# Kernel optimization log

Measured on AMD Instinct MI355X. Metric: run time of the kernel, lower is better.

## Reference

```python
import jax, jax.numpy as jnp
import numpy as np

N_NODES = 100000
N_EDGES = 3200000
IN_SIZE = 256
HID_SIZE = 256
OUT_SIZE = 64


def setup_inputs() -> dict:
    key = jax.random.key(0)
    ks = jax.random.split(key, 8)
    X = jax.random.normal(ks[0], (N_NODES, IN_SIZE), dtype=jnp.float32)
    edge_vals = jax.random.uniform(ks[1], (N_EDGES,), dtype=jnp.float32)
    # xavier-uniform-ish init for weights
    lim1 = float(np.sqrt(6.0 / (IN_SIZE + HID_SIZE)))
    W1 = jax.random.uniform(ks[2], (IN_SIZE, HID_SIZE), minval=-lim1, maxval=lim1, dtype=jnp.float32)
    b1 = jnp.zeros((HID_SIZE,), dtype=jnp.float32)
    lim2 = float(np.sqrt(6.0 / (HID_SIZE + OUT_SIZE)))
    W2 = jax.random.uniform(ks[3], (HID_SIZE, OUT_SIZE), minval=-lim2, maxval=lim2, dtype=jnp.float32)
    b2 = jnp.zeros((OUT_SIZE,), dtype=jnp.float32)
    row = jnp.sort(jax.random.randint(ks[4], (N_EDGES,), 0, N_NODES, dtype=jnp.int32))
    col = jax.random.randint(ks[5], (N_EDGES,), 0, N_NODES, dtype=jnp.int32)
    return {"X": X, "edge_vals": edge_vals, "W1": W1, "b1": b1,
            "W2": W2, "b2": b2, "row": row, "col": col}


def reference(X, edge_vals, W1, b1, W2, b2, row, col):
    """2-layer GCN (eval mode, dropout = identity).

    A is a sparse NxN matrix in COO form: A[row[e], col[e]] = edge_vals[e].
    Layer: relu(A @ (X @ W1) + b1); output: A @ (h @ W2) + b2.
    """
    n = X.shape[0]

    def spmm(dense):  # (A @ dense): gather columns, scale, segment-sum over rows
        gathered = edge_vals[:, None] * dense[col]        # [E, F]
        return jax.ops.segment_sum(gathered, row, num_segments=n)

    h = spmm(X @ W1) + b1          # [N, HID]
    h = jax.nn.relu(h)
    out = spmm(h @ W2) + b2        # [N, OUT]
    return out
```

## Files before the change

kernel.cpp:

```cpp
#include <hip/hip_runtime.h>


constexpr int IN_SIZE = 256;
constexpr int HID = 256;
constexpr int OUTF = 64;

typedef __bf16 bf16x8 __attribute__((ext_vector_type(8)));
typedef float f32x4 __attribute__((ext_vector_type(4)));

__device__ __forceinline__ ushort f2b(float f) {
    uint u = __float_as_uint(f);
    uint r = (u + 0x7fffu + ((u >> 16) & 1u)) >> 16;
    return (ushort)r;
}

__device__ __forceinline__ void fma4(float* a, uint word, float w) {
    a[0] += w * (float)(word & 0xffu);
    a[1] += w * (float)((word >> 8) & 0xffu);
    a[2] += w * (float)((word >> 16) & 0xffu);
    a[3] += w * (float)(word >> 24);
}

__device__ __forceinline__ bf16x8 pack8(float4 a, float4 b) {
    union { uint4 u; bf16x8 h; } cv;
    cv.u.x = (uint)f2b(a.x) | ((uint)f2b(a.y) << 16);
    cv.u.y = (uint)f2b(a.z) | ((uint)f2b(a.w) << 16);
    cv.u.z = (uint)f2b(b.x) | ((uint)f2b(b.y) << 16);
    cv.u.w = (uint)f2b(b.z) | ((uint)f2b(b.w) << 16);
    return cv.h;
}

__global__ void setup_kernel(const int* __restrict__ row, int* __restrict__ rp,
                             const float* __restrict__ W1, ushort* __restrict__ W1T,
                             const float* __restrict__ W2, ushort* __restrict__ W2T,
                             int n, int E, int rpB) {
    int b = blockIdx.x;
    if (b < rpB) {
        int i = b * 256 + threadIdx.x;
        if (i > n) return;
        int lo = 0, hi = E;
        while (lo < hi) {
            int mid = (lo + hi) >> 1;
            if (row[mid] < i) lo = mid + 1; else hi = mid;
        }
        rp[i] = lo;
    } else if (b < rpB + 256) {
        int nn = b - rpB;
        int k = threadIdx.x;
        W1T[(size_t)nn * 256 + k] = f2b(W1[(size_t)k * 256 + nn]);
    } else {
        int nn = b - rpB - 256;
        int k = threadIdx.x;
        W2T[(size_t)nn * 256 + k] = f2b(W2[(size_t)k * 64 + nn]);
    }
}

__global__ void prep_edges(const float* __restrict__ vals, const int* __restrict__ col,
                           const float* __restrict__ s, int2* __restrict__ ew,
                           int E, int shift) {
    int e = blockIdx.x * 256 + threadIdx.x;
    if (e >= E) return;
    int c = col[e];
    ew[e] = make_int2(c << shift, __float_as_int(vals[e] * s[c]));
}

__global__ __launch_bounds__(512)
void gemm1_q(const float* __restrict__ A, const ushort* __restrict__ Bt,
             unsigned char* __restrict__ Q, float* __restrict__ s1, int M) {
    __shared__ uint4 Wlds[8192];
    const int tid = threadIdx.x;
    const int wave = tid >> 6, lane = tid & 63;
    const int quad = lane >> 4, l = lane & 15;
    const int wr = wave >> 2, wc = wave & 3;
    const int m0 = blockIdx.x * 128;

    for (int i = tid; i < 8192; i += 512) {
        uint4 v = ((const uint4*)Bt)[i];
        Wlds[(i & ~31) | ((i & 31) ^ ((i >> 5) & 7))] = v;
    }
    __syncthreads();

    size_t abase[4];
#pragma unroll
    for (int mt = 0; mt < 4; ++mt) {
        int r = min(m0 + wr * 64 + mt * 16 + l, M - 1);
        abase[mt] = (size_t)r * 256 + quad * 8;
    }

    f32x4 acc[4][4] = {};
    float4 ra[4], rb[4];
#pragma unroll
    for (int mt = 0; mt < 4; ++mt) {
        ra[mt] = *(const float4*)(A + abase[mt]);
        rb[mt] = *(const float4*)(A + abase[mt] + 4);
    }

#pragma unroll
    for (int kstep = 0; kstep < 8; ++kstep) {
        bf16x8 af[4];
#pragma unroll
        for (int mt = 0; mt < 4; ++mt)
            af[mt] = pack8(ra[mt], rb[mt]);
        if (kstep < 7) {
#pragma unroll
            for (int mt = 0; mt < 4; ++mt) {
                ra[mt] = *(const float4*)(A + abase[mt] + (kstep + 1) * 32);
                rb[mt] = *(const float4*)(A + abase[mt] + (kstep + 1) * 32 + 4);
            }
        }
        bf16x8 bfr[4];
#pragma unroll
        for (int nt = 0; nt < 4; ++nt) {
            int c = wc * 64 + nt * 16 + l;
            int idx = c * 32 + (((kstep << 2) + quad) ^ (c & 7));
            bfr[nt] = *(const bf16x8*)&Wlds[idx];
        }
#pragma unroll
        for (int mt = 0; mt < 4; ++mt)
#pragma unroll
            for (int nt = 0; nt < 4; ++nt)
                acc[mt][nt] = __builtin_amdgcn_mfma_f32_16x16x32_bf16(
                    af[mt], bfr[nt], acc[mt][nt], 0, 0, 0);
    }

    __syncthreads();
    float* red = (float*)Wlds;
    float* fin = red + 512;

    float rmax[4][4];
#pragma unroll
    for (int mt = 0; mt < 4; ++mt)
#pragma unroll
        for (int reg = 0; reg < 4; ++reg) {
            float m = 0.f;
#pragma unroll
            for (int nt = 0; nt < 4; ++nt)
                m = fmaxf(m, fabsf(acc[mt][nt][reg]));
            rmax[mt][reg] = m;
        }
#pragma unroll
    for (int s = 1; s <= 8; s <<= 1)
#pragma unroll
        for (int mt = 0; mt < 4; ++mt)
#pragma unroll
            for (int reg = 0; reg < 4; ++reg)
                rmax[mt][reg] = fmaxf(rmax[mt][reg], __shfl_xor(rmax[mt][reg], s));
    if (l < 4) {
#pragma unroll
        for (int mt = 0; mt < 4; ++mt)
            red[wc * 128 + wr * 64 + mt * 16 + quad * 4 + l] = rmax[mt][l];
    }
    __syncthreads();
    if (tid < 128) {
        float m = fmaxf(fmaxf(red[tid], red[128 + tid]),
                        fmaxf(red[256 + tid], red[384 + tid]));
        fin[tid] = m;
        int r = m0 + tid;
        if (r < M) s1[r] = m * (1.f / 127.f);
    }
    __syncthreads();

#pragma unroll
    for (int mt = 0; mt < 4; ++mt)
#pragma unroll
        for (int reg = 0; reg < 4; ++reg) {
            int rl = wr * 64 + mt * 16 + quad * 4 + reg;
            int r = m0 + rl;
            if (r >= M) continue;
            float m = fin[rl];
            float inv = m > 0.f ? 127.f / m : 0.f;
#pragma unroll
            for (int nt = 0; nt < 4; ++nt) {
                int c = wc * 64 + nt * 16 + l;
                Q[(size_t)r * 256 + c] =
                    (unsigned char)((int)rintf(acc[mt][nt][reg] * inv) + 128);
            }
        }
}

__global__ __launch_bounds__(256, 4)
void gemm2_q(const ushort* __restrict__ A, const ushort* __restrict__ Bt,
             unsigned char* __restrict__ Q, float* __restrict__ s2, int M) {
    __shared__ uint4 Wlds[2048];
    const int tid = threadIdx.x;
    const int wave = tid >> 6, lane = tid & 63;
    const int quad = lane >> 4, l = lane & 15;
    const int r0 = blockIdx.x * 128 + wave * 32;

    for (int i = tid; i < 2048; i += 256) {
        uint4 v = ((const uint4*)Bt)[i];
        Wlds[(i & ~31) | ((i & 31) ^ ((i >> 5) & 7))] = v;
    }
    __syncthreads();

    size_t abase[2];
#pragma unroll
    for (int mt = 0; mt < 2; ++mt) {
        int r = min(r0 + mt * 16 + l, M - 1);
        abase[mt] = (size_t)r * 256 + quad * 8;
    }

    f32x4 acc[2][4] = {};
    uint4 ra[2];
#pragma unroll
    for (int mt = 0; mt < 2; ++mt)
        ra[mt] = *(const uint4*)(A + abase[mt]);

#pragma unroll
    for (int kstep = 0; kstep < 8; ++kstep) {
        bf16x8 af[2];
#pragma unroll
        for (int mt = 0; mt < 2; ++mt)
            af[mt] = *(const bf16x8*)&ra[mt];
        if (kstep < 7) {
#pragma unroll
            for (int mt = 0; mt < 2; ++mt)
                ra[mt] = *(const uint4*)(A + abase[mt] + (kstep + 1) * 32);
        }
        bf16x8 bfr[4];
#pragma unroll
        for (int nt = 0; nt < 4; ++nt) {
            int c = nt * 16 + l;
            int idx = c * 32 + (((kstep << 2) + quad) ^ (c & 7));
            bfr[nt] = *(const bf16x8*)&Wlds[idx];
        }
#pragma unroll
        for (int mt = 0; mt < 2; ++mt)
#pragma unroll
            for (int nt = 0; nt < 4; ++nt)
                acc[mt][nt] = __builtin_amdgcn_mfma_f32_16x16x32_bf16(
                    af[mt], bfr[nt], acc[mt][nt], 0, 0, 0);
    }

    float rmax[2][4];
#pragma unroll
    for (int mt = 0; mt < 2; ++mt)
#pragma unroll
        for (int reg = 0; reg < 4; ++reg) {
            float m = fmaxf(fabsf(acc[mt][0][reg]), fabsf(acc[mt][1][reg]));
            m = fmaxf(m, fabsf(acc[mt][2][reg]));
            m = fmaxf(m, fabsf(acc[mt][3][reg]));
            rmax[mt][reg] = m;
        }
#pragma unroll
    for (int s = 1; s <= 8; s <<= 1)
#pragma unroll
        for (int mt = 0; mt < 2; ++mt)
#pragma unroll
            for (int reg = 0; reg < 4; ++reg)
                rmax[mt][reg] = fmaxf(rmax[mt][reg], __shfl_xor(rmax[mt][reg], s));

#pragma unroll
    for (int mt = 0; mt < 2; ++mt)
#pragma unroll
        for (int reg = 0; reg < 4; ++reg) {
            int r = r0 + mt * 16 + quad * 4 + reg;
            if (r >= M) continue;
            float m = rmax[mt][reg];
            if (l == 0) s2[r] = m * (1.f / 127.f);
            float inv = m > 0.f ? 127.f / m : 0.f;
#pragma unroll
            for (int nt = 0; nt < 4; ++nt) {
                int c = nt * 16 + l;
                Q[(size_t)r * 64 + c] =
                    (unsigned char)((int)rintf(acc[mt][nt][reg] * inv) + 128);
            }
        }
}

__global__ __launch_bounds__(256)
void spmm1_q(const unsigned char* __restrict__ Q, const int2* __restrict__ ew,
             const int* __restrict__ rp, const float* __restrict__ bias,
             ushort* __restrict__ H, int n) {
    const int wave = threadIdx.x >> 6;
    const int lane = threadIdx.x & 63;
    const int node = blockIdx.x * 4 + wave;
    if (node >= n) return;
    const int e0 = rp[node], e1 = rp[node + 1];
    const int g = lane >> 4;
    const int fb = (lane & 15) * 16;

    float acc[16] = {};
    float sumw = 0.f;
    int e = e0;
    for (; e + 16 <= e1; e += 16) {
#pragma unroll
        for (int u = 0; u < 4; ++u) {
            int2 m = ew[e + u * 4 + g];
            float w = __int_as_float(m.y);
            uint4 qv = *(const uint4*)(Q + (size_t)(uint)m.x + fb);
            sumw += w;
            fma4(&acc[0], qv.x, w);
            fma4(&acc[4], qv.y, w);
            fma4(&acc[8], qv.z, w);
            fma4(&acc[12], qv.w, w);
        }
    }
    for (; e < e1; e += 4) {
        int idx = e + g;
        int2 m = ew[idx];
        bool ok = idx < e1;
        uint off = ok ? (uint)m.x : 0u;
        float w = ok ? __int_as_float(m.y) : 0.f;
        uint4 qv = *(const uint4*)(Q + (size_t)off + fb);
        sumw += w;
        fma4(&acc[0], qv.x, w);
        fma4(&acc[4], qv.y, w);
        fma4(&acc[8], qv.z, w);
        fma4(&acc[12], qv.w, w);
    }

#pragma unroll
    for (int s = 16; s <= 32; s <<= 1) {
#pragma unroll
        for (int j = 0; j < 16; ++j)
            acc[j] += __shfl_xor(acc[j], s);
        sumw += __shfl_xor(sumw, s);
    }

    if (g == 0) {
        const int f0 = (lane & 15) * 16;
        float4 b0 = *(const float4*)(bias + f0);
        float4 b1 = *(const float4*)(bias + f0 + 4);
        float4 b2 = *(const float4*)(bias + f0 + 8);
        float4 b3 = *(const float4*)(bias + f0 + 12);
        float bb[16] = {b0.x, b0.y, b0.z, b0.w, b1.x, b1.y, b1.z, b1.w,
                        b2.x, b2.y, b2.z, b2.w, b3.x, b3.y, b3.z, b3.w};
        float fix = -128.f * sumw;
        ushort r[16];
#pragma unroll
        for (int j = 0; j < 16; ++j)
            r[j] = f2b(fmaxf(acc[j] + fix + bb[j], 0.f));
        uint4 w0, w1;
        w0.x = (uint)r[0] | ((uint)r[1] << 16);
        w0.y = (uint)r[2] | ((uint)r[3] << 16);
        w0.z = (uint)r[4] | ((uint)r[5] << 16);
        w0.w = (uint)r[6] | ((uint)r[7] << 16);
        w1.x = (uint)r[8] | ((uint)r[9] << 16);
        w1.y = (uint)r[10] | ((uint)r[11] << 16);
        w1.z = (uint)r[12] | ((uint)r[13] << 16);
        w1.w = (uint)r[14] | ((uint)r[15] << 16);
        *(uint4*)(H + (size_t)node * 256 + f0) = w0;
        *(uint4*)(H + (size_t)node * 256 + f0 + 8) = w1;
    }
}

__global__ __launch_bounds__(256)
void spmm2_q(const unsigned char* __restrict__ Q, const int2* __restrict__ ew,
             const int* __restrict__ rp, const float* __restrict__ bias,
             float* __restrict__ O, int n) {
    const int wave = threadIdx.x >> 6;
    const int lane = threadIdx.x & 63;
    const int node = blockIdx.x * 4 + wave;
    if (node >= n) return;
    const int e0 = rp[node], e1 = rp[node + 1];
    const int g = lane >> 3;
    const int fb = (lane & 7) * 8;

    float acc[8] = {};
    float sumw = 0.f;
    int e = e0;
    for (; e + 16 <= e1; e += 16) {
#pragma unroll
        for (int u = 0; u < 2; ++u) {
            int2 m = ew[e + u * 8 + g];
            float w = __int_as_float(m.y);
            uint2 qv = *(const uint2*)(Q + (size_t)(uint)m.x + fb);
            sumw += w;
            fma4(&acc[0], qv.x, w);
            fma4(&acc[4], qv.y, w);
        }
    }
    for (; e < e1; e += 8) {
        int idx = e + g;
        int2 m = ew[idx];
        bool ok = idx < e1;
        uint off = ok ? (uint)m.x : 0u;
        float w = ok ? __int_as_float(m.y) : 0.f;
        uint2 qv = *(const uint2*)(Q + (size_t)off + fb);
        sumw += w;
        fma4(&acc[0], qv.x, w);
        fma4(&acc[4], qv.y, w);
    }

#pragma unroll
    for (int s = 8; s <= 32; s <<= 1) {
#pragma unroll
        for (int j = 0; j < 8; ++j)
            acc[j] += __shfl_xor(acc[j], s);
        sumw += __shfl_xor(sumw, s);
    }

    if (g == 0) {
        const int f0 = (lane & 7) * 8;
        float4 b0 = *(const float4*)(bias + f0);
        float4 b1 = *(const float4*)(bias + f0 + 4);
        float fix = -128.f * sumw;
        float4 o0, o1;
        o0.x = acc[0] + fix + b0.x;
        o0.y = acc[1] + fix + b0.y;
        o0.z = acc[2] + fix + b0.z;
        o0.w = acc[3] + fix + b0.w;
        o1.x = acc[4] + fix + b1.x;
        o1.y = acc[5] + fix + b1.y;
        o1.z = acc[6] + fix + b1.z;
        o1.w = acc[7] + fix + b1.w;
        *(float4*)(O + (size_t)node * 64 + f0) = o0;
        *(float4*)(O + (size_t)node * 64 + f0 + 4) = o1;
    }
}

static inline size_t alignup(size_t x) { return (x + 255) & ~(size_t)255; }

extern "C" void kernel_launch(void* const* d_in, const int* in_sizes, int n_in,
                              void* d_out, int out_size, void* d_ws, size_t ws_size,
                              hipStream_t stream) {
    const float* X  = (const float*)d_in[0];
    const float* ev = (const float*)d_in[1];
    const float* W1 = (const float*)d_in[2];
    const float* b1 = (const float*)d_in[3];
    const float* W2 = (const float*)d_in[4];
    const float* b2 = (const float*)d_in[5];
    const int*  row = (const int*)d_in[6];
    const int*  col = (const int*)d_in[7];
    float* out = (float*)d_out;

    const int n = in_sizes[0] / IN_SIZE;
    const int E = in_sizes[1];

    char* p = (char*)d_ws;
    ushort* H    = (ushort*)p; p += alignup((size_t)n * HID * 2);
    unsigned char* Q1 = (unsigned char*)p; p += alignup((size_t)n * HID);
    float*  s1   = (float*)p;  p += alignup((size_t)n * 4);
    unsigned char* Q2 = (unsigned char*)p; p += alignup((size_t)n * OUTF);
    float*  s2   = (float*)p;  p += alignup((size_t)n * 4);
    ushort* W1T  = (ushort*)p; p += alignup((size_t)IN_SIZE * HID * 2);
    ushort* W2T  = (ushort*)p; p += alignup((size_t)HID * OUTF * 2);
    int*    rp   = (int*)p;    p += alignup((size_t)(n + 1) * 4);
    int2*   ewb  = (int2*)p;   p += alignup((size_t)(E + 16) * 8);

    const int rpB = (n + 1 + 255) / 256;
    setup_kernel<<<rpB + 256 + 64, 256, 0, stream>>>(row, rp, W1, W1T, W2, W2T,
                                                     n, E, rpB);

    gemm1_q<<<(n + 127) / 128, 512, 0, stream>>>(X, W1T, Q1, s1, n);

    prep_edges<<<(E + 255) / 256, 256, 0, stream>>>(ev, col, s1, ewb, E, 8);

    spmm1_q<<<(n + 3) / 4, 256, 0, stream>>>(Q1, ewb, rp, b1, H, n);

    gemm2_q<<<(n + 127) / 128, 256, 0, stream>>>(H, W2T, Q2, s2, n);

    prep_edges<<<(E + 255) / 256, 256, 0, stream>>>(ev, col, s2, ewb, E, 6);

    spmm2_q<<<(n + 3) / 4, 256, 0, stream>>>(Q2, ewb, rp, b2, out, n);
}
```

Before: 484.5 us.

## Retile gemm1 to 1024-thread blocks, deepen A prefetch, split spmm1 launch

gemm1_q now uses 1024-thread blocks covering 256 rows, with each wave computing a 32x128 tile instead of 64x64. The W1 LDS load is amortized over twice as many rows, and B fragments are loaded one at a time to reduce register pressure. Both GEMMs now prefetch A two k-steps ahead to hide global load latency. spmm1 is split into two launches over node halves, which adds a launch with no clear benefit, possibly for cache locality or as an experiment.

```diff
diff --git a/kernel.cpp b/kernel.cpp
--- a/kernel.cpp
+++ b/kernel.cpp
@@ -64,96 +64,96 @@
     ew[e] = make_int2(c << shift, __float_as_int(vals[e] * s[c]));
 }
 
-__global__ __launch_bounds__(512)
+__global__ __launch_bounds__(1024)
 void gemm1_q(const float* __restrict__ A, const ushort* __restrict__ Bt,
              unsigned char* __restrict__ Q, float* __restrict__ s1, int M) {
     __shared__ uint4 Wlds[8192];
     const int tid = threadIdx.x;
     const int wave = tid >> 6, lane = tid & 63;
     const int quad = lane >> 4, l = lane & 15;
-    const int wr = wave >> 2, wc = wave & 3;
-    const int m0 = blockIdx.x * 128;
-
-    for (int i = tid; i < 8192; i += 512) {
+    const int wr = wave >> 1, wc = wave & 1;
+    const int m0 = blockIdx.x * 256;
+
+    for (int i = tid; i < 8192; i += 1024) {
         uint4 v = ((const uint4*)Bt)[i];
         Wlds[(i & ~31) | ((i & 31) ^ ((i >> 5) & 7))] = v;
     }
     __syncthreads();
 
-    size_t abase[4];
-#pragma unroll
-    for (int mt = 0; mt < 4; ++mt) {
-        int r = min(m0 + wr * 64 + mt * 16 + l, M - 1);
+    size_t abase[2];
+#pragma unroll
+    for (int mt = 0; mt < 2; ++mt) {
+        int r = min(m0 + wr * 32 + mt * 16 + l, M - 1);
         abase[mt] = (size_t)r * 256 + quad * 8;
     }
 
-    f32x4 acc[4][4] = {};
-    float4 ra[4], rb[4];
-#pragma unroll
-    for (int mt = 0; mt < 4; ++mt) {
-        ra[mt] = *(const float4*)(A + abase[mt]);
-        rb[mt] = *(const float4*)(A + abase[mt] + 4);
+    f32x4 acc[2][8] = {};
+    float4 ra0[2], rb0[2], ra1[2], rb1[2];
+#pragma unroll
+    for (int mt = 0; mt < 2; ++mt) {
+        ra0[mt] = *(const float4*)(A + abase[mt]);
+        rb0[mt] = *(const float4*)(A + abase[mt] + 4);
+        ra1[mt] = *(const float4*)(A + abase[mt] + 32);
+        rb1[mt] = *(const float4*)(A + abase[mt] + 36);
     }
 
 #pragma unroll
     for (int kstep = 0; kstep < 8; ++kstep) {
-        bf16x8 af[4];
-#pragma unroll
-        for (int mt = 0; mt < 4; ++mt)
-            af[mt] = pack8(ra[mt], rb[mt]);
-        if (kstep < 7) {
-#pragma unroll
-            for (int mt = 0; mt < 4; ++mt) {
-                ra[mt] = *(const float4*)(A + abase[mt] + (kstep + 1) * 32);
-                rb[mt] = *(const float4*)(A + abase[mt] + (kstep + 1) * 32 + 4);
+        bf16x8 af[2];
+#pragma unroll
+        for (int mt = 0; mt < 2; ++mt)
+            af[mt] = pack8(ra0[mt], rb0[mt]);
+#pragma unroll
+        for (int mt = 0; mt < 2; ++mt) { ra0[mt] = ra1[mt]; rb0[mt] = rb1[mt]; }
+        if (kstep < 6) {
+#pragma unroll
+            for (int mt = 0; mt < 2; ++mt) {
+                ra1[mt] = *(const float4*)(A + abase[mt] + (kstep + 2) * 32);
+                rb1[mt] = *(const float4*)(A + abase[mt] + (kstep + 2) * 32 + 4);
             }
         }
-        bf16x8 bfr[4];
-#pragma unroll
-        for (int nt = 0; nt < 4; ++nt) {
-            int c = wc * 64 + nt * 16 + l;
+#pragma unroll
+        for (int nt = 0; nt < 8; ++nt) {
+            int c = wc * 128 + nt * 16 + l;
             int idx = c * 32 + (((kstep << 2) + quad) ^ (c & 7));
-            bfr[nt] = *(const bf16x8*)&Wlds[idx];
-        }
-#pragma unroll
-        for (int mt = 0; mt < 4; ++mt)
-#pragma unroll
-            for (int nt = 0; nt < 4; ++nt)
+            bf16x8 bfr = *(const bf16x8*)&Wlds[idx];
+#pragma unroll
+            for (int mt = 0; mt < 2; ++mt)
                 acc[mt][nt] = __builtin_amdgcn_mfma_f32_16x16x32_bf16(
-                    af[mt], bfr[nt], acc[mt][nt], 0, 0, 0);
+                    af[mt], bfr, acc[mt][nt], 0, 0, 0);
+        }
     }
 
     __syncthreads();
     float* red = (float*)Wlds;
     float* fin = red + 512;
 
-    float rmax[4][4];
-#pragma unroll
-    for (int mt = 0; mt < 4; ++mt)
+    float rmax[2][4];
+#pragma unroll
+    for (int mt = 0; mt < 2; ++mt)
 #pragma unroll
         for (int reg = 0; reg < 4; ++reg) {
             float m = 0.f;
 #pragma unroll
-            for (int nt = 0; nt < 4; ++nt)
+            for (int nt = 0; nt < 8; ++nt)
                 m = fmaxf(m, fabsf(acc[mt][nt][reg]));
             rmax[mt][reg] = m;
         }
 #pragma unroll
     for (int s = 1; s <= 8; s <<= 1)
 #pragma unroll
-        for (int mt = 0; mt < 4; ++mt)
+        for (int mt = 0; mt < 2; ++mt)
 #pragma unroll
             for (int reg = 0; reg < 4; ++reg)
                 rmax[mt][reg] = fmaxf(rmax[mt][reg], __shfl_xor(rmax[mt][reg], s));
     if (l < 4) {
 #pragma unroll
-        for (int mt = 0; mt < 4; ++mt)
-            red[wc * 128 + wr * 64 + mt * 16 + quad * 4 + l] = rmax[mt][l];
+        for (int mt = 0; mt < 2; ++mt)
+            red[wc * 256 + wr * 32 + mt * 16 + quad * 4 + l] = rmax[mt][l];
     }
     __syncthreads();
-    if (tid < 128) {
-        float m = fmaxf(fmaxf(red[tid], red[128 + tid]),
-                        fmaxf(red[256 + tid], red[384 + tid]));
+    if (tid < 256) {
+        float m = fmaxf(red[tid], red[256 + tid]);
         fin[tid] = m;
         int r = m0 + tid;
         if (r < M) s1[r] = m * (1.f / 127.f);
@@ -161,17 +161,17 @@
     __syncthreads();
 
 #pragma unroll
-    for (int mt = 0; mt < 4; ++mt)
+    for (int mt = 0; mt < 2; ++mt)
 #pragma unroll
         for (int reg = 0; reg < 4; ++reg) {
-            int rl = wr * 64 + mt * 16 + quad * 4 + reg;
+            int rl = wr * 32 + mt * 16 + quad * 4 + reg;
             int r = m0 + rl;
             if (r >= M) continue;
             float m = fin[rl];
             float inv = m > 0.f ? 127.f / m : 0.f;
 #pragma unroll
-            for (int nt = 0; nt < 4; ++nt) {
-                int c = wc * 64 + nt * 16 + l;
+            for (int nt = 0; nt < 8; ++nt) {
+                int c = wc * 128 + nt * 16 + l;
                 Q[(size_t)r * 256 + c] =
                     (unsigned char)((int)rintf(acc[mt][nt][reg] * inv) + 128);
             }
@@ -201,21 +201,25 @@
     }
 
     f32x4 acc[2][4] = {};
-    uint4 ra[2];
-#pragma unroll
-    for (int mt = 0; mt < 2; ++mt)
-        ra[mt] = *(const uint4*)(A + abase[mt]);
+    uint4 ra0[2], ra1[2];
+#pragma unroll
+    for (int mt = 0; mt < 2; ++mt) {
+        ra0[mt] = *(const uint4*)(A + abase[mt]);
+        ra1[mt] = *(const uint4*)(A + abase[mt] + 32);
+    }
 
 #pragma unroll
     for (int kstep = 0; kstep < 8; ++kstep) {
         bf16x8 af[2];
 #pragma unroll
         for (int mt = 0; mt < 2; ++mt)
-            af[mt] = *(const bf16x8*)&ra[mt];
-        if (kstep < 7) {
+            af[mt] = *(const bf16x8*)&ra0[mt];
+#pragma unroll
+        for (int mt = 0; mt < 2; ++mt) ra0[mt] = ra1[mt];
+        if (kstep < 6) {
 #pragma unroll
             for (int mt = 0; mt < 2; ++mt)
-                ra[mt] = *(const uint4*)(A + abase[mt] + (kstep + 1) * 32);
+                ra1[mt] = *(const uint4*)(A + abase[mt] + (kstep + 2) * 32);
         }
         bf16x8 bfr[4];
 #pragma unroll
@@ -271,11 +275,11 @@
 __global__ __launch_bounds__(256)
 void spmm1_q(const unsigned char* __restrict__ Q, const int2* __restrict__ ew,
              const int* __restrict__ rp, const float* __restrict__ bias,
-             ushort* __restrict__ H, int n) {
+             ushort* __restrict__ H, int node0, int nend) {
     const int wave = threadIdx.x >> 6;
     const int lane = threadIdx.x & 63;
-    const int node = blockIdx.x * 4 + wave;
-    if (node >= n) return;
+    const int node = node0 + blockIdx.x * 4 + wave;
+    if (node >= nend) return;
     const int e0 = rp[node], e1 = rp[node + 1];
     const int g = lane >> 4;
     const int fb = (lane & 15) * 16;
@@ -443,11 +447,13 @@
     setup_kernel<<<rpB + 256 + 64, 256, 0, stream>>>(row, rp, W1, W1T, W2, W2T,
                                                      n, E, rpB);
 
-    gemm1_q<<<(n + 127) / 128, 512, 0, stream>>>(X, W1T, Q1, s1, n);
+    gemm1_q<<<(n + 255) / 256, 1024, 0, stream>>>(X, W1T, Q1, s1, n);
 
     prep_edges<<<(E + 255) / 256, 256, 0, stream>>>(ev, col, s1, ewb, E, 8);
 
-    spmm1_q<<<(n + 3) / 4, 256, 0, stream>>>(Q1, ewb, rp, b1, H, n);
+    const int half = (n + 1) / 2;
+    spmm1_q<<<(half + 3) / 4, 256, 0, stream>>>(Q1, ewb, rp, b1, H, 0, half);
+    spmm1_q<<<(n - half + 3) / 4, 256, 0, stream>>>(Q1, ewb, rp, b1, H, half, n);
 
     gemm2_q<<<(n + 127) / 128, 256, 0, stream>>>(H, W2T, Q2, s2, n);
 
```

New measurement: 448.0 us. 1.08x faster.
